# Kernel optimization log

Measured on AMD Instinct MI355X. Metric: run time of the kernel, lower is better.

## Reference

```python
import jax, jax.numpy as jnp
import numpy as np

EPS = 1e-5
K = 16  # neighbors

def bn(x, g, b):
    # BatchNorm in training mode: stats over all axes except the last (channel)
    ax = tuple(range(x.ndim - 1))
    m = x.mean(ax, keepdims=True)
    v = x.var(ax, keepdims=True)
    return g * (x - m) * jax.lax.rsqrt(v + EPS) + b

def setup_inputs() -> dict:
    key = jax.random.key(0)
    ks = jax.random.split(key, 12)
    B, N, M, C, D = 2, 16384, 4096, 32, 64
    H = D // 2
    p = lambda k, s: jax.random.normal(k, s, dtype=jnp.float32) * 0.1
    inp = {}
    inp["xyz"] = jax.random.normal(ks[0], (B, N, 3), dtype=jnp.float32)
    inp["feats"] = jax.random.normal(ks[1], (B, C, N), dtype=jnp.float32)
    inp["sample_idx"] = jax.random.randint(ks[2], (B, M), 0, N, dtype=jnp.int32)
    # RelativePosEncoder mlp: Conv2d(10, H, 1) + BN
    inp["W_pos"] = p(ks[3], (10, H)); inp["b_pos"] = jnp.zeros(H); inp["g_pos"] = jnp.ones(H); inp["be_pos"] = jnp.zeros(H)
    # feature_mlp: Conv2d(C, H, 1) + BN
    inp["W_feat"] = p(ks[4], (C, H)); inp["b_feat"] = jnp.zeros(H); inp["g_feat"] = jnp.ones(H); inp["be_feat"] = jnp.zeros(H)
    # attention score mlp: Conv2d(D, D, 1, bias=False)
    inp["W_score"] = p(ks[5], (D, D))
    # out_mlp: Conv1d(D, D, 1, bias=False) + BN
    inp["W_out"] = p(ks[6], (D, D)); inp["g_out"] = jnp.ones(D); inp["be_out"] = jnp.zeros(D)
    # LFA shortcut: Conv1d(C, D, 1, bias=False) + BN
    inp["W_sc1"] = p(ks[7], (C, D)); inp["g_sc1"] = jnp.ones(D); inp["be_sc1"] = jnp.zeros(D)
    # unit shortcut: Conv1d(C, D, 1, bias=False) + BN
    inp["W_sc2"] = p(ks[8], (C, D)); inp["g_sc2"] = jnp.ones(D); inp["be_sc2"] = jnp.zeros(D)
    return inp

def reference(xyz, feats, sample_idx,
              W_pos, b_pos, g_pos, be_pos,
              W_feat, b_feat, g_feat, be_feat,
              W_score,
              W_out, g_out, be_out,
              W_sc1, g_sc1, be_sc1,
              W_sc2, g_sc2, be_sc2):
    B, C, N = feats.shape
    featsT = jnp.transpose(feats, (0, 2, 1))                    # [B,N,C]
    xyz_ds = jnp.take_along_axis(xyz, sample_idx[:, :, None], axis=1)  # [B,M,3]
    # KNN: squared distances are monotone in cdist -> same topk indices
    d2 = jnp.sum((xyz_ds[:, :, None, :] - xyz[:, None, :, :]) ** 2, axis=-1)  # [B,M,N]
    _, knn_idx = jax.lax.top_k(-d2, K)                           # [B,M,K]
    gather = jax.vmap(lambda pts, idx: pts[idx])
    neigh_xyz = gather(xyz, knn_idx)                             # [B,M,K,3]
    neigh_feats = gather(featsT, knn_idx)                        # [B,M,K,C]
    center_feats = jnp.take_along_axis(featsT, sample_idx[:, :, None], axis=1)  # [B,M,C]
    # relative position encoding
    center = jnp.broadcast_to(xyz_ds[:, :, None, :], neigh_xyz.shape)
    rel = xyz_ds[:, :, None, :] - neigh_xyz                      # [B,M,K,3]
    dist = jnp.linalg.norm(rel, axis=-1, keepdims=True)          # [B,M,K,1]
    posf = jnp.concatenate([center, neigh_xyz, rel, dist], axis=-1)  # [B,M,K,10]
    pos_feats = jax.nn.relu(bn(posf @ W_pos + b_pos, g_pos, be_pos))       # [B,M,K,H]
    feat_feats = jax.nn.relu(bn(neigh_feats @ W_feat + b_feat, g_feat, be_feat))  # [B,M,K,H]
    combined = jnp.concatenate([feat_feats, pos_feats], axis=-1)  # [B,M,K,D]
    # attention pooling: softmax over the K (neighbor) axis
    scores = jax.nn.softmax(combined @ W_score, axis=2)
    pooled = jnp.sum(scores * combined, axis=2)                  # [B,M,D]
    out = jax.nn.relu(bn(pooled @ W_out, g_out, be_out))         # [B,M,D]
    sc1 = bn(jnp.mean(neigh_feats, axis=2) @ W_sc1, g_sc1, be_sc1)
    f_lfa = out + sc1
    f_sc = bn(center_feats @ W_sc2, g_sc2, be_sc2)
    y = jax.nn.relu(f_lfa + f_sc)                                # [B,M,D]
    return xyz_ds, jnp.transpose(y, (0, 2, 1)), sample_idx
```

## Files before the change

kernel.cpp:

```cpp
#include <hip/hip_runtime.h>
#include <math.h>

#define BB 2
#define NN 16384
#define MM 4096
#define C_IN 32
#define D_DIM 64
#define H_DIM 32
#define KNB 16
#define EPSV 1e-5f
#define FLT_BIG 3.0e38f
#define CAPK 128
#define NSPL 4
#define SPTS (NN / NSPL)

#define SPOS_SUM 0
#define SPOS_SQ 32
#define SFEAT_SUM 64
#define SFEAT_SQ 96
#define SSC1_SUM 128
#define SSC1_SQ 192
#define SSC2_SUM 256
#define SSC2_SQ 320
#define SOUT_SUM 384
#define SOUT_SQ 448
#define STATS_LEN 512
#define PA_W 384
#define PB_W 128
#define NBLK (BB * MM / 4)

__device__ __forceinline__ int clampi_r19(int v, int lo, int hi) {
    return v < lo ? lo : (v > hi ? hi : v);
}

__global__ __launch_bounds__(256) void prep_r19(const float* __restrict__ feats,
                                                const float* __restrict__ xyz,
                                                const int* __restrict__ sample_idx,
                                                float* __restrict__ featsT,
                                                float* __restrict__ xyz4,
                                                float* __restrict__ stats,
                                                float* __restrict__ out) {
    __shared__ float tile[C_IN][65];
    const int tid = threadIdx.x;
    const int b = blockIdx.x >> 8;
    const int n0 = (blockIdx.x & 255) * 64;
#pragma unroll
    for (int it = 0; it < 8; ++it) {
        int c = (tid >> 6) + 4 * it;
        int n = tid & 63;
        tile[c][n] = feats[((size_t)b * C_IN + c) * NN + n0 + n];
    }
    int e = blockIdx.x * 256 + tid;
    if (e < STATS_LEN) stats[e] = 0.f;
    if (e < BB * NN) {
        float x = xyz[e * 3 + 0], y = xyz[e * 3 + 1], z = xyz[e * 3 + 2];
        xyz4[e * 4 + 0] = x;
        xyz4[e * 4 + 1] = y;
        xyz4[e * 4 + 2] = z;
        xyz4[e * 4 + 3] = x * x + y * y + z * z;
    }
    if (e < BB * MM) {
        int bb2 = e >> 12;
        int sidx = clampi_r19(sample_idx[e], 0, NN - 1);
        const float* p = xyz + (size_t)(bb2 * NN + sidx) * 3;
        out[e * 3 + 0] = p[0];
        out[e * 3 + 1] = p[1];
        out[e * 3 + 2] = p[2];
        out[BB * MM * 3 + BB * D_DIM * MM + e] = (float)sample_idx[e];
    }
    __syncthreads();
#pragma unroll
    for (int it = 0; it < 8; ++it) {
        int c = tid & 31;
        int nn = (tid >> 5) + 8 * it;
        featsT[((size_t)b * NN + n0 + nn) * C_IN + c] = tile[c][nn];
    }
}

__device__ void knn_fullsplit_r19(const float* __restrict__ base4, int n0,
                                  float m2x, float m2y, float m2z, int lane,
                                  float* __restrict__ outd, int* __restrict__ outi) {
    float d2v[KNB]; int iv[KNB];
#pragma unroll
    for (int i = 0; i < KNB; i++) { d2v[i] = FLT_BIG; iv[i] = 0x7FFFFFFF; }
    float curmax = FLT_BIG; int amax = 0;
    for (int t = 0; t < SPTS / 64; ++t) {
        int n = n0 + lane + t * 64;
        const float4 p = *reinterpret_cast<const float4*>(base4 + (size_t)n * 4);
        float d2 = fmaf(p.x, m2x, p.w);
        d2 = fmaf(p.y, m2y, d2);
        d2 = fmaf(p.z, m2z, d2);
        if (d2 < curmax) {
#pragma unroll
            for (int i = 0; i < KNB; i++)
                if (i == amax) { d2v[i] = d2; iv[i] = n; }
            curmax = d2v[0]; amax = 0;
#pragma unroll
            for (int i = 1; i < KNB; i++)
                if (d2v[i] > curmax) { curmax = d2v[i]; amax = i; }
        }
    }
#pragma unroll
    for (int i = 0; i < KNB; i++) {
#pragma unroll
        for (int j = 0; j < KNB - 1; j++) {
            bool sw = (d2v[j] > d2v[j + 1]) ||
                      (d2v[j] == d2v[j + 1] && iv[j] > iv[j + 1]);
            if (sw) {
                float td = d2v[j]; d2v[j] = d2v[j + 1]; d2v[j + 1] = td;
                int   ti = iv[j];  iv[j]  = iv[j + 1];  iv[j + 1]  = ti;
            }
        }
    }
    float myd = FLT_BIG; int myidx = 0x7FFFFFFF;
#pragma unroll 1
    for (int r = 0; r < KNB; r++) {
        float cv = d2v[0]; int cid = iv[0]; int ml = lane;
#pragma unroll
        for (int off = 32; off > 0; off >>= 1) {
            float ov = __shfl_xor(cv, off);
            int   oid = __shfl_xor(cid, off);
            int   ol = __shfl_xor(ml, off);
            bool take = (ov < cv) || (ov == cv && oid < cid);
            cv = take ? ov : cv; cid = take ? oid : cid; ml = take ? ol : ml;
        }
        if (lane == r) { myd = cv; myidx = cid; }
        if (lane == ml) {
#pragma unroll
            for (int i = 0; i < KNB - 1; i++) { d2v[i] = d2v[i + 1]; iv[i] = iv[i + 1]; }
            d2v[KNB - 1] = FLT_BIG; iv[KNB - 1] = 0x7FFFFFFF;
        }
    }
    if (lane < KNB) { outd[lane] = myd; outi[lane] = myidx; }
}

__global__ __launch_bounds__(256) void knn_r19(const float* __restrict__ xyz4,
                                               const int* __restrict__ sample_idx,
                                               float* __restrict__ cand_d,
                                               int* __restrict__ cand_i) {
    __shared__ float bufd[16][CAPK];
    __shared__ int   bufi[16][CAPK];
    const int tid = threadIdx.x;
    const int w = tid >> 6, lane = tid & 63;
    const int split = blockIdx.x & (NSPL - 1);
    const int qgrp = blockIdx.x >> 2;
    const int qbase = qgrp * 16 + w * 4;
    const int b = qbase >> 12;
    const int n0 = split * SPTS;
    const float* base4 = xyz4 + (size_t)b * NN * 4;
    const float4* p4 = reinterpret_cast<const float4*>(base4) + n0 + lane;

    float m2x[4], m2y[4], m2z[4], md[4], v16[4];
#pragma unroll
    for (int j = 0; j < 4; j++) {
        int s = clampi_r19(sample_idx[qbase + j], 0, NN - 1);
        m2x[j] = -2.f * base4[(size_t)s * 4 + 0];
        m2y[j] = -2.f * base4[(size_t)s * 4 + 1];
        m2z[j] = -2.f * base4[(size_t)s * 4 + 2];
        md[j] = FLT_BIG;
    }
#pragma unroll 8
    for (int it = 0; it < SPTS / 64; ++it) {
        const float4 p = p4[(size_t)it * 64];
#pragma unroll
        for (int j = 0; j < 4; j++) {
            float t = fmaf(p.x, m2x[j], p.w);
            t = fmaf(p.y, m2y[j], t);
            t = fmaf(p.z, m2z[j], t);
            md[j] = fminf(md[j], t);
        }
    }
    {
        float sv[4];
#pragma unroll
        for (int j = 0; j < 4; j++) sv[j] = md[j];
#pragma unroll
        for (int k = 2; k <= 64; k <<= 1) {
#pragma unroll
            for (int j2 = k >> 1; j2 >= 1; j2 >>= 1) {
                const bool want_min = (((lane & j2) == 0) == ((lane & k) == 0));
#pragma unroll
                for (int j = 0; j < 4; j++) {
                    float ov = __shfl_xor(sv[j], j2);
                    float mn = fminf(sv[j], ov);
                    float mx = fmaxf(sv[j], ov);
                    sv[j] = want_min ? mn : mx;
                }
            }
        }
#pragma unroll
        for (int j = 0; j < 4; j++) v16[j] = __shfl(sv[j], KNB - 1);
    }
    int cnt[4] = {0, 0, 0, 0};
#pragma unroll 4
    for (int it = 0; it < SPTS / 64; ++it) {
        const float4 p = p4[(size_t)it * 64];
        const int n = n0 + lane + it * 64;
#pragma unroll
        for (int j = 0; j < 4; j++) {
            float t = fmaf(p.x, m2x[j], p.w);
            t = fmaf(p.y, m2y[j], t);
            t = fmaf(p.z, m2z[j], t);
            bool pred = (t <= v16[j]);
            unsigned long long bal = __ballot(pred);
            if (bal) {
                int pre = __builtin_amdgcn_mbcnt_hi((unsigned)(bal >> 32),
                          __builtin_amdgcn_mbcnt_lo((unsigned)bal, 0u));
                int pos = cnt[j] + pre;
                if (pred && pos < CAPK) {
                    bufd[w * 4 + j][pos] = t;
                    bufi[w * 4 + j][pos] = n;
                }
                cnt[j] += __popcll(bal);
            }
        }
    }
    {
        float dv[4]; int ivv[4];
#pragma unroll
        for (int j = 0; j < 4; j++) {
            const int qi = w * 4 + j;
            bool valid = (cnt[j] <= 64) && (lane < cnt[j]);
            dv[j]  = valid ? bufd[qi][lane] : FLT_BIG;
            ivv[j] = valid ? bufi[qi][lane] : 0x7FFFFFFF;
        }
#pragma unroll
        for (int k = 2; k <= 64; k <<= 1) {
#pragma unroll
            for (int j2 = k >> 1; j2 >= 1; j2 >>= 1) {
                const bool want_min = (((lane & j2) == 0) == ((lane & k) == 0));
#pragma unroll
                for (int j = 0; j < 4; j++) {
                    float od = __shfl_xor(dv[j], j2);
                    int   oi = __shfl_xor(ivv[j], j2);
                    bool mine_less = (dv[j] < od) || (dv[j] == od && ivv[j] < oi);
                    bool keep = (mine_less == want_min);
                    dv[j]  = keep ? dv[j]  : od;
                    ivv[j] = keep ? ivv[j] : oi;
                }
            }
        }
#pragma unroll 1
        for (int j = 0; j < 4; j++) {
            const int qi = w * 4 + j;
            const int q = qbase + j;
            float* outd = cand_d + ((size_t)q * NSPL + split) * KNB;
            int*   outi = cand_i + ((size_t)q * NSPL + split) * KNB;
            if (cnt[j] <= 64) {
                if (lane < KNB) { outd[lane] = dv[j]; outi[lane] = ivv[j]; }
            } else if (cnt[j] <= CAPK) {
#pragma unroll 1
                for (int half = 0; half < 2; ++half) {
                    int i = lane + 64 * half;
                    if (i < cnt[j]) {
                        float di = bufd[qi][i]; int xi = bufi[qi][i];
                        int rank = 0;
                        for (int t = 0; t < cnt[j]; ++t) {
                            float dt = bufd[qi][t]; int xt = bufi[qi][t];
                            rank += (dt < di || (dt == di && xt < xi)) ? 1 : 0;
                        }
                        if (rank < KNB) { outd[rank] = di; outi[rank] = xi; }
                    }
                }
            } else {
                knn_fullsplit_r19(base4, n0, m2x[j], m2y[j], m2z[j], lane, outd, outi);
            }
        }
    }
}

__device__ __forceinline__ void prebn_r19(const float (*posf)[12], const float (*nf)[C_IN],
                                          int k, int h,
                                          const float* __restrict__ W_pos, const float* __restrict__ b_pos,
                                          const float* __restrict__ W_feat, const float* __restrict__ b_feat,
                                          float* a_out, float* f_out) {
    float4 p0 = *reinterpret_cast<const float4*>(&posf[k][0]);
    float4 p1 = *reinterpret_cast<const float4*>(&posf[k][4]);
    float p8 = posf[k][8], p9 = posf[k][9];
    float a = b_pos[h];
    a += p0.x * W_pos[0 * H_DIM + h]; a += p0.y * W_pos[1 * H_DIM + h];
    a += p0.z * W_pos[2 * H_DIM + h]; a += p0.w * W_pos[3 * H_DIM + h];
    a += p1.x * W_pos[4 * H_DIM + h]; a += p1.y * W_pos[5 * H_DIM + h];
    a += p1.z * W_pos[6 * H_DIM + h]; a += p1.w * W_pos[7 * H_DIM + h];
    a += p8 * W_pos[8 * H_DIM + h];   a += p9 * W_pos[9 * H_DIM + h];
    float f = b_feat[h];
#pragma unroll
    for (int j4 = 0; j4 < C_IN / 4; ++j4) {
        float4 c = *reinterpret_cast<const float4*>(&nf[k][j4 * 4]);
        f += c.x * W_feat[(j4 * 4 + 0) * H_DIM + h];
        f += c.y * W_feat[(j4 * 4 + 1) * H_DIM + h];
        f += c.z * W_feat[(j4 * 4 + 2) * H_DIM + h];
        f += c.w * W_feat[(j4 * 4 + 3) * H_DIM + h];
    }
    *a_out = a; *f_out = f;
}

__global__ __launch_bounds__(256) void stageA_r19(const float* __restrict__ xyz4,
                                                  const int* __restrict__ sample_idx,
                                                  const float* __restrict__ featsT,
                                                  const float* __restrict__ cand_d,
                                                  const int* __restrict__ cand_i,
                                                  const float* __restrict__ W_pos, const float* __restrict__ b_pos,
                                                  const float* __restrict__ W_feat, const float* __restrict__ b_feat,
                                                  const float* __restrict__ W_sc1, const float* __restrict__ W_sc2,
                                                  float* __restrict__ combpre,
                                                  float* __restrict__ sc1_pre, float* __restrict__ sc2_pre,
                                                  float* __restrict__ partialsA) {
    __shared__ int   idxs[4][KNB];
    __shared__ float sd[4][64];
    __shared__ int   si[4][64];
    __shared__ __align__(16) float posf[4][KNB][12];
    __shared__ __align__(16) float nf[4][KNB][C_IN];
    __shared__ float meanf[4][C_IN];
    __shared__ float centerf[4][C_IN];
    __shared__ float posS[4][H_DIM], posQ[4][H_DIM], featS[4][H_DIM], featQ[4][H_DIM];
    __shared__ float s1S[4][D_DIM], s1Q[4][D_DIM], s2S[4][D_DIM], s2Q[4][D_DIM];
    const int tid = threadIdx.x;
    const int w = tid >> 6, lane = tid & 63;
    const int q = blockIdx.x * 4 + w;
    const int b = q >> 12;
    const int sidx = clampi_r19(sample_idx[q], 0, NN - 1);
    const float* base4 = xyz4 + (size_t)b * NN * 4;

    float d = cand_d[(size_t)q * 64 + lane];
    int   i = cand_i[(size_t)q * 64 + lane];
    float qx = base4[(size_t)sidx * 4 + 0];
    float qy = base4[(size_t)sidx * 4 + 1];
    float qz = base4[(size_t)sidx * 4 + 2];
    float cfv = 0.f;
    if (lane < C_IN) cfv = featsT[((size_t)b * NN + sidx) * C_IN + lane];

    {
        sd[w][lane] = d; si[w][lane] = i;
        __syncthreads();
        int rank = 0;
#pragma unroll
        for (int t = 0; t < 64; ++t) {
            float dt = sd[w][t]; int it = si[w][t];
            rank += (dt < d || (dt == d && it < i)) ? 1 : 0;
        }
        if (rank < KNB) idxs[w][rank] = i;
        if (lane < C_IN) centerf[w][lane] = cfv;
        __syncthreads();
    }

    if (lane < KNB) {
        int idx = clampi_r19(idxs[w][lane], 0, NN - 1);
        float nx = base4[(size_t)idx * 4 + 0];
        float ny = base4[(size_t)idx * 4 + 1];
        float nz = base4[(size_t)idx * 4 + 2];
        float rx = qx - nx, ry = qy - ny, rz = qz - nz;
        float dist = sqrtf(rx * rx + ry * ry + rz * rz);
        posf[w][lane][0] = qx; posf[w][lane][1] = qy; posf[w][lane][2] = qz;
        posf[w][lane][3] = nx; posf[w][lane][4] = ny; posf[w][lane][5] = nz;
        posf[w][lane][6] = rx; posf[w][lane][7] = ry; posf[w][lane][8] = rz;
        posf[w][lane][9] = dist; posf[w][lane][10] = 0.f; posf[w][lane][11] = 0.f;
    }
    __syncthreads();
    const float* fT = featsT + (size_t)b * NN * C_IN;
#pragma unroll
    for (int ii = 0; ii < 2; ++ii) {
        int e4 = lane + 64 * ii;
        int k = e4 >> 3, c4 = e4 & 7;
        const float4 v = *reinterpret_cast<const float4*>(fT + (size_t)idxs[w][k] * C_IN + c4 * 4);
        *reinterpret_cast<float4*>(&nf[w][k][c4 * 4]) = v;
    }
    __syncthreads();

    const int h = lane & 31;
    float sP = 0.f, qP = 0.f, sF = 0.f, qF = 0.f;
    float* cp = combpre + (size_t)q * (KNB * D_DIM);
#pragma unroll
    for (int i2 = 0; i2 < 8; i2++) {
        int k = ((lane + 64 * i2) >> 5);
        float a, f;
        prebn_r19(posf[w], nf[w], k, h, W_pos, b_pos, W_feat, b_feat, &a, &f);
        sP += a; qP += a * a;
        sF += f; qF += f * f;
        cp[k * D_DIM + h] = f;
        cp[k * D_DIM + H_DIM + h] = a;
    }
    sP += __shfl_xor(sP, 32); qP += __shfl_xor(qP, 32);
    sF += __shfl_xor(sF, 32); qF += __shfl_xor(qF, 32);
    if (lane < H_DIM) {
        posS[w][h] = sP; posQ[w][h] = qP; featS[w][h] = sF; featQ[w][h] = qF;
    }
    if (lane < C_IN) {
        float s = 0.f;
#pragma unroll
        for (int k = 0; k < KNB; k++) s += nf[w][k][lane];
        meanf[w][lane] = s * (1.f / (float)KNB);
    }
    __syncthreads();
    {
        float a = 0.f, c2 = 0.f;
#pragma unroll
        for (int j = 0; j < C_IN; j++) {
            a  += meanf[w][j]   * W_sc1[j * D_DIM + lane];
            c2 += centerf[w][j] * W_sc2[j * D_DIM + lane];
        }
        sc1_pre[(size_t)q * D_DIM + lane] = a;
        sc2_pre[(size_t)q * D_DIM + lane] = c2;
        s1S[w][lane] = a;  s1Q[w][lane] = a * a;
        s2S[w][lane] = c2; s2Q[w][lane] = c2 * c2;
    }
    __syncthreads();
    float* row = partialsA + (size_t)blockIdx.x * PA_W;
    if (tid < H_DIM) {
        row[SPOS_SUM + tid]  = posS[0][tid] + posS[1][tid] + posS[2][tid] + posS[3][tid];
        row[SPOS_SQ + tid]   = posQ[0][tid] + posQ[1][tid] + posQ[2][tid] + posQ[3][tid];
        row[SFEAT_SUM + tid] = featS[0][tid] + featS[1][tid] + featS[2][tid] + featS[3][tid];
        row[SFEAT_SQ + tid]  = featQ[0][tid] + featQ[1][tid] + featQ[2][tid] + featQ[3][tid];
    } else if (tid >= 64 && tid < 128) {
        int dd = tid - 64;
        row[SSC1_SUM + dd] = s1S[0][dd] + s1S[1][dd] + s1S[2][dd] + s1S[3][dd];
        row[SSC1_SQ + dd]  = s1Q[0][dd] + s1Q[1][dd] + s1Q[2][dd] + s1Q[3][dd];
    } else if (tid >= 128 && tid < 192) {
        int dd = tid - 128;
        row[SSC2_SUM + dd] = s2S[0][dd] + s2S[1][dd] + s2S[2][dd] + s2S[3][dd];
        row[SSC2_SQ + dd]  = s2Q[0][dd] + s2Q[1][dd] + s2Q[2][dd] + s2Q[3][dd];
    }
}

#define NRSPLIT 64
__global__ __launch_bounds__(256) void reduce_r19(const float* __restrict__ partials,
                                                  int rows, int width,
                                                  float* __restrict__ stats_out) {
    const int wchunks = (width + 255) / 256;
    const int wi = blockIdx.x % wchunks;
    const int pi = blockIdx.x / wchunks;
    const int c = wi * 256 + threadIdx.x;
    if (c >= width) return;
    const int per = rows / NRSPLIT;
    const int p0 = pi * per;
    float s = 0.f;
    for (int p = p0; p < p0 + per; ++p) s += partials[(size_t)p * width + c];
    atomicAdd(&stats_out[c], s);
}

__global__ __launch_bounds__(256) void stageB_r19(const float* __restrict__ combpre,
                                                  const float* __restrict__ g_pos, const float* __restrict__ be_pos,
                                                  const float* __restrict__ g_feat, const float* __restrict__ be_feat,
                                                  const float* __restrict__ W_score, const float* __restrict__ W_out,
                                                  const float* __restrict__ stats,
                                                  float* __restrict__ out_pre,
                                                  float* __restrict__ partialsB) {
    __shared__ __align__(16) float comb[4][KNB][D_DIM];
    __shared__ float scl[D_DIM], shf[D_DIM];
    __shared__ float pooled[4][D_DIM];
    __shared__ float oS[4][D_DIM], oQ[4][D_DIM];
    const int tid = threadIdx.x;
    const int w = tid >> 6, lane = tid & 63;
    const int q = blockIdx.x * 4 + w;

    if (tid < D_DIM) {
        const float inv1 = 1.f / (float)(BB * MM * KNB);
        float mean, var, g, bb;
        if (tid < H_DIM) {
            mean = stats[SFEAT_SUM + tid] * inv1;
            var  = fmaxf(stats[SFEAT_SQ + tid] * inv1 - mean * mean, 0.f);
            g = g_feat[tid]; bb = be_feat[tid];
        } else {
            int h = tid - H_DIM;
            mean = stats[SPOS_SUM + h] * inv1;
            var  = fmaxf(stats[SPOS_SQ + h] * inv1 - mean * mean, 0.f);
            g = g_pos[h]; bb = be_pos[h];
        }
        float s = g * rsqrtf(var + EPSV);
        scl[tid] = s;
        shf[tid] = bb - mean * s;
    }
    __syncthreads();

    const float4* src = reinterpret_cast<const float4*>(combpre + (size_t)blockIdx.x * 4 * KNB * D_DIM);
#pragma unroll
    for (int i = 0; i < 4; ++i) {
        int f = tid + 256 * i;
        int qloc = f >> 8;
        int k = (f >> 4) & 15;
        int j4 = f & 15;
        float4 v = src[f];
        int j = j4 * 4;
        v.x = fmaxf(v.x * scl[j + 0] + shf[j + 0], 0.f);
        v.y = fmaxf(v.y * scl[j + 1] + shf[j + 1], 0.f);
        v.z = fmaxf(v.z * scl[j + 2] + shf[j + 2], 0.f);
        v.w = fmaxf(v.w * scl[j + 3] + shf[j + 3], 0.f);
        *reinterpret_cast<float4*>(&comb[qloc][k][j]) = v;
    }
    __syncthreads();

    const int d = lane;
    float s[KNB];
#pragma unroll
    for (int k = 0; k < KNB; k++) s[k] = 0.f;
#pragma unroll 4
    for (int j4 = 0; j4 < D_DIM / 4; ++j4) {
        float w0 = W_score[(j4 * 4 + 0) * D_DIM + d];
        float w1 = W_score[(j4 * 4 + 1) * D_DIM + d];
        float w2 = W_score[(j4 * 4 + 2) * D_DIM + d];
        float w3 = W_score[(j4 * 4 + 3) * D_DIM + d];
#pragma unroll
        for (int k = 0; k < KNB; k++) {
            float4 cb = *reinterpret_cast<const float4*>(&comb[w][k][j4 * 4]);
            s[k] += cb.x * w0 + cb.y * w1 + cb.z * w2 + cb.w * w3;
        }
    }
    float mx = s[0];
#pragma unroll
    for (int k = 1; k < KNB; k++) mx = fmaxf(mx, s[k]);
    float sum = 0.f;
#pragma unroll
    for (int k = 0; k < KNB; k++) { s[k] = __expf(s[k] - mx); sum += s[k]; }
    float inv = 1.f / sum;
    float pv = 0.f;
#pragma unroll
    for (int k = 0; k < KNB; k++) pv += s[k] * inv * comb[w][k][d];
    pooled[w][d] = pv;
    __syncthreads();
    float o = 0.f;
#pragma unroll
    for (int dd = 0; dd < D_DIM; dd++) o += pooled[w][dd] * W_out[dd * D_DIM + d];
    out_pre[(size_t)q * D_DIM + d] = o;
    oS[w][d] = o; oQ[w][d] = o * o;
    __syncthreads();
    float* row = partialsB + (size_t)blockIdx.x * PB_W;
    if (tid < D_DIM) {
        row[tid] = oS[0][tid] + oS[1][tid] + oS[2][tid] + oS[3][tid];
    } else if (tid < 2 * D_DIM) {
        int dd = tid - D_DIM;
        row[D_DIM + dd] = oQ[0][dd] + oQ[1][dd] + oQ[2][dd] + oQ[3][dd];
    }
}

__global__ __launch_bounds__(256) void final_r19(const float* __restrict__ out_pre,
                                                 const float* __restrict__ sc1_pre,
                                                 const float* __restrict__ sc2_pre,
                                                 const float* __restrict__ stats,
                                                 const float* __restrict__ g_out, const float* __restrict__ be_out,
                                                 const float* __restrict__ g_sc1, const float* __restrict__ be_sc1,
                                                 const float* __restrict__ g_sc2, const float* __restrict__ be_sc2,
                                                 float* __restrict__ out) {
    __shared__ float yt[64][65];
    const int tid = threadIdx.x;
    const int blk = blockIdx.x;
    const int b = blk >> 6;
    const int m0 = (blk & 63) * 64;
    const int d = tid & 63;

    const float invn = 1.f / (float)(BB * MM);
    float mo = stats[SOUT_SUM + d] * invn;
    float vo = fmaxf(stats[SOUT_SQ + d] * invn - mo * mo, 0.f);
    float so = g_out[d] * rsqrtf(vo + EPSV);
    float oo = be_out[d] - mo * so;
    float m1 = stats[SSC1_SUM + d] * invn;
    float v1 = fmaxf(stats[SSC1_SQ + d] * invn - m1 * m1, 0.f);
    float s1 = g_sc1[d] * rsqrtf(v1 + EPSV);
    float o1 = be_sc1[d] - m1 * s1;
    float m2 = stats[SSC2_SUM + d] * invn;
    float v2 = fmaxf(stats[SSC2_SQ + d] * invn - m2 * m2, 0.f);
    float s2 = g_sc2[d] * rsqrtf(v2 + EPSV);
    float o2 = be_sc2[d] - m2 * s2;

#pragma unroll
    for (int p = 0; p < 16; p++) {
        int ml = (tid >> 6) + 4 * p;
        size_t q = (size_t)b * MM + m0 + ml;
        float x_out = fmaxf(out_pre[q * D_DIM + d] * so + oo, 0.f);
        float x1 = sc1_pre[q * D_DIM + d] * s1 + o1;
        float x2 = sc2_pre[q * D_DIM + d] * s2 + o2;
        yt[ml][d] = fmaxf(x_out + x1 + x2, 0.f);
    }
    __syncthreads();
#pragma unroll
    for (int p = 0; p < 16; p++) {
        int dr = (tid >> 6) + 4 * p;
        int mc = tid & 63;
        out[BB * MM * 3 + (size_t)b * (D_DIM * MM) + (size_t)dr * MM + m0 + mc] = yt[mc][dr];
    }
}

extern "C" void kernel_launch(void* const* d_in, const int* in_sizes, int n_in,
                              void* d_out, int out_size, void* d_ws, size_t ws_size,
                              hipStream_t stream) {
    const float* xyz        = (const float*)d_in[0];
    const float* feats      = (const float*)d_in[1];
    const int*   sample_idx = (const int*)d_in[2];
    const float* W_pos  = (const float*)d_in[3];
    const float* b_pos  = (const float*)d_in[4];
    const float* g_pos  = (const float*)d_in[5];
    const float* be_pos = (const float*)d_in[6];
    const float* W_feat  = (const float*)d_in[7];
    const float* b_feat  = (const float*)d_in[8];
    const float* g_feat  = (const float*)d_in[9];
    const float* be_feat = (const float*)d_in[10];
    const float* W_score = (const float*)d_in[11];
    const float* W_out  = (const float*)d_in[12];
    const float* g_out  = (const float*)d_in[13];
    const float* be_out = (const float*)d_in[14];
    const float* W_sc1  = (const float*)d_in[15];
    const float* g_sc1  = (const float*)d_in[16];
    const float* be_sc1 = (const float*)d_in[17];
    const float* W_sc2  = (const float*)d_in[18];
    const float* g_sc2  = (const float*)d_in[19];
    const float* be_sc2 = (const float*)d_in[20];

    float* out = (float*)d_out;
    float* ws = (float*)d_ws;

    float* featsT    = ws;
    float* xyz4      = featsT + 1048576;
    float* sc1_pre   = xyz4 + 131072;
    float* sc2_pre   = sc1_pre + 524288;
    float* out_pre   = sc2_pre + 524288;
    float* stats     = out_pre + 524288;
    float* partialsA = stats + STATS_LEN;
    float* partialsB = partialsA + NBLK * PA_W;
    float* cand_d    = partialsB + NBLK * PB_W;
    int*   cand_i    = (int*)(cand_d + (size_t)BB * MM * NSPL * KNB);
    float* combpre   = (float*)(cand_i + (size_t)BB * MM * NSPL * KNB);

    prep_r19<<<BB * (NN / 64), 256, 0, stream>>>(feats, xyz, sample_idx,
                                                 featsT, xyz4, stats, out);

    knn_r19<<<(BB * MM / 16) * NSPL, 256, 0, stream>>>(xyz4, sample_idx, cand_d, cand_i);

    stageA_r19<<<NBLK, 256, 0, stream>>>(xyz4, sample_idx, featsT, cand_d, cand_i,
                                         W_pos, b_pos, W_feat, b_feat, W_sc1, W_sc2,
                                         combpre, sc1_pre, sc2_pre, partialsA);
    reduce_r19<<<2 * NRSPLIT, 256, 0, stream>>>(partialsA, NBLK, PA_W, stats);

    stageB_r19<<<NBLK, 256, 0, stream>>>(combpre,
                                         g_pos, be_pos, g_feat, be_feat,
                                         W_score, W_out, stats, out_pre, partialsB);
    reduce_r19<<<1 * NRSPLIT, 256, 0, stream>>>(partialsB, NBLK, PB_W, stats + SOUT_SUM);

    final_r19<<<BB * (MM / 64), 256, 0, stream>>>(out_pre, sc1_pre, sc2_pre, stats,
                                                  g_out, be_out, g_sc1, be_sc1, g_sc2, be_sc2, out);
}
```

Measured before the change: 251.9 us.

## Use packed float2 math in KNN and MLPs, replace rank-merge with bitonic shuffle

Adds a pair-interleaved xyz layout, stored in the combpre workspace, so the KNN distance scan and candidate filter handle two points per lane using packed float2 FMA. stageA swaps the shared-memory O(64) rank selection of 16 neighbours out of 4 sorted runs for a wave-level bitonic merge via shuffles. It also drops several __syncthreads, caches W_pos/W_feat in registers as float2 pairs, and packs the stageB score matmul into float2 FMAs. Risks: the xyz8 buffer aliases combpre, the removed barriers may break cross-wave shared-memory reads, and the ballot ordering now differs for candidate collection.

```diff
diff --git a/kernel.cpp b/kernel.cpp
--- a/kernel.cpp
+++ b/kernel.cpp
@@ -29,15 +29,22 @@
 #define PB_W 128
 #define NBLK (BB * MM / 4)
 
-__device__ __forceinline__ int clampi_r19(int v, int lo, int hi) {
+typedef float f32x2 __attribute__((ext_vector_type(2)));
+
+__device__ __forceinline__ f32x2 mk2_r20(float a, float b) {
+    f32x2 r; r.x = a; r.y = b; return r;
+}
+
+__device__ __forceinline__ int clampi_r20(int v, int lo, int hi) {
     return v < lo ? lo : (v > hi ? hi : v);
 }
 
-__global__ __launch_bounds__(256) void prep_r19(const float* __restrict__ feats,
+__global__ __launch_bounds__(256) void prep_r20(const float* __restrict__ feats,
                                                 const float* __restrict__ xyz,
                                                 const int* __restrict__ sample_idx,
                                                 float* __restrict__ featsT,
                                                 float* __restrict__ xyz4,
+                                                float* __restrict__ xyz8,
                                                 float* __restrict__ stats,
                                                 float* __restrict__ out) {
     __shared__ float tile[C_IN][65];
@@ -54,14 +61,20 @@
     if (e < STATS_LEN) stats[e] = 0.f;
     if (e < BB * NN) {
         float x = xyz[e * 3 + 0], y = xyz[e * 3 + 1], z = xyz[e * 3 + 2];
+        float w = x * x + y * y + z * z;
         xyz4[e * 4 + 0] = x;
         xyz4[e * 4 + 1] = y;
         xyz4[e * 4 + 2] = z;
-        xyz4[e * 4 + 3] = x * x + y * y + z * z;
+        xyz4[e * 4 + 3] = w;
+        size_t pb = ((size_t)(e >> 1)) * 8 + (e & 1);
+        xyz8[pb + 0] = x;
+        xyz8[pb + 2] = y;
+        xyz8[pb + 4] = z;
+        xyz8[pb + 6] = w;
     }
     if (e < BB * MM) {
         int bb2 = e >> 12;
-        int sidx = clampi_r19(sample_idx[e], 0, NN - 1);
+        int sidx = clampi_r20(sample_idx[e], 0, NN - 1);
         const float* p = xyz + (size_t)(bb2 * NN + sidx) * 3;
         out[e * 3 + 0] = p[0];
         out[e * 3 + 1] = p[1];
@@ -77,7 +90,7 @@
     }
 }
 
-__device__ void knn_fullsplit_r19(const float* __restrict__ base4, int n0,
+__device__ void knn_fullsplit_r20(const float* __restrict__ base4, int n0,
                                   float m2x, float m2y, float m2z, int lane,
                                   float* __restrict__ outd, int* __restrict__ outi) {
     float d2v[KNB]; int iv[KNB];
@@ -134,7 +147,8 @@
     if (lane < KNB) { outd[lane] = myd; outi[lane] = myidx; }
 }
 
-__global__ __launch_bounds__(256) void knn_r19(const float* __restrict__ xyz4,
+__global__ __launch_bounds__(256) void knn_r20(const float* __restrict__ xyz4,
+                                               const float* __restrict__ xyz8,
                                                const int* __restrict__ sample_idx,
                                                float* __restrict__ cand_d,
                                                int* __restrict__ cand_i) {
@@ -148,28 +162,39 @@
     const int b = qbase >> 12;
     const int n0 = split * SPTS;
     const float* base4 = xyz4 + (size_t)b * NN * 4;
-    const float4* p4 = reinterpret_cast<const float4*>(base4) + n0 + lane;
-
-    float m2x[4], m2y[4], m2z[4], md[4], v16[4];
+    const float* base8 = xyz8 + (size_t)b * NN * 4;
+    const float4* q8 = reinterpret_cast<const float4*>(base8) + ((size_t)(n0 >> 1) + lane) * 2;
+
+    f32x2 m2x2[4], m2y2[4], m2z2[4], md2[4];
+    float md[4], v16[4];
 #pragma unroll
     for (int j = 0; j < 4; j++) {
-        int s = clampi_r19(sample_idx[qbase + j], 0, NN - 1);
-        m2x[j] = -2.f * base4[(size_t)s * 4 + 0];
-        m2y[j] = -2.f * base4[(size_t)s * 4 + 1];
-        m2z[j] = -2.f * base4[(size_t)s * 4 + 2];
-        md[j] = FLT_BIG;
-    }
-#pragma unroll 8
-    for (int it = 0; it < SPTS / 64; ++it) {
-        const float4 p = p4[(size_t)it * 64];
+        int s = clampi_r20(sample_idx[qbase + j], 0, NN - 1);
+        float mx = -2.f * base4[(size_t)s * 4 + 0];
+        float my = -2.f * base4[(size_t)s * 4 + 1];
+        float mz = -2.f * base4[(size_t)s * 4 + 2];
+        m2x2[j] = mk2_r20(mx, mx);
+        m2y2[j] = mk2_r20(my, my);
+        m2z2[j] = mk2_r20(mz, mz);
+        md2[j] = mk2_r20(FLT_BIG, FLT_BIG);
+    }
+#pragma unroll 4
+    for (int it = 0; it < SPTS / 128; ++it) {
+        const float4 A = q8[(size_t)it * 128];
+        const float4 B = q8[(size_t)it * 128 + 1];
+        f32x2 x2 = mk2_r20(A.x, A.y), y2 = mk2_r20(A.z, A.w);
+        f32x2 z2 = mk2_r20(B.x, B.y), w2 = mk2_r20(B.z, B.w);
 #pragma unroll
         for (int j = 0; j < 4; j++) {
-            float t = fmaf(p.x, m2x[j], p.w);
-            t = fmaf(p.y, m2y[j], t);
-            t = fmaf(p.z, m2z[j], t);
-            md[j] = fminf(md[j], t);
-        }
-    }
+            f32x2 t2 = x2 * m2x2[j] + w2;
+            t2 = y2 * m2y2[j] + t2;
+            t2 = z2 * m2z2[j] + t2;
+            md2[j].x = fminf(md2[j].x, t2.x);
+            md2[j].y = fminf(md2[j].y, t2.y);
+        }
+    }
+#pragma unroll
+    for (int j = 0; j < 4; j++) md[j] = fminf(md2[j].x, md2[j].y);
     {
         float sv[4];
 #pragma unroll
@@ -193,25 +218,31 @@
     }
     int cnt[4] = {0, 0, 0, 0};
 #pragma unroll 4
-    for (int it = 0; it < SPTS / 64; ++it) {
-        const float4 p = p4[(size_t)it * 64];
-        const int n = n0 + lane + it * 64;
+    for (int it = 0; it < SPTS / 128; ++it) {
+        const float4 A = q8[(size_t)it * 128];
+        const float4 B = q8[(size_t)it * 128 + 1];
+        f32x2 x2 = mk2_r20(A.x, A.y), y2 = mk2_r20(A.z, A.w);
+        f32x2 z2 = mk2_r20(B.x, B.y), w2 = mk2_r20(B.z, B.w);
+        const int ne = n0 + (it << 7) + (lane << 1);
 #pragma unroll
         for (int j = 0; j < 4; j++) {
-            float t = fmaf(p.x, m2x[j], p.w);
-            t = fmaf(p.y, m2y[j], t);
-            t = fmaf(p.z, m2z[j], t);
-            bool pred = (t <= v16[j]);
-            unsigned long long bal = __ballot(pred);
-            if (bal) {
-                int pre = __builtin_amdgcn_mbcnt_hi((unsigned)(bal >> 32),
-                          __builtin_amdgcn_mbcnt_lo((unsigned)bal, 0u));
-                int pos = cnt[j] + pre;
-                if (pred && pos < CAPK) {
-                    bufd[w * 4 + j][pos] = t;
-                    bufi[w * 4 + j][pos] = n;
-                }
-                cnt[j] += __popcll(bal);
+            f32x2 t2 = x2 * m2x2[j] + w2;
+            t2 = y2 * m2y2[j] + t2;
+            t2 = z2 * m2z2[j] + t2;
+            bool h0 = (t2.x <= v16[j]);
+            bool h1 = (t2.y <= v16[j]);
+            unsigned long long b0 = __ballot(h0);
+            unsigned long long b1 = __ballot(h1);
+            if (b0 | b1) {
+                int base = cnt[j];
+                int c0 = __popcll(b0);
+                int p0 = base + __builtin_amdgcn_mbcnt_hi((unsigned)(b0 >> 32),
+                             __builtin_amdgcn_mbcnt_lo((unsigned)b0, 0u));
+                int p1 = base + c0 + __builtin_amdgcn_mbcnt_hi((unsigned)(b1 >> 32),
+                             __builtin_amdgcn_mbcnt_lo((unsigned)b1, 0u));
+                if (h0 && p0 < CAPK) { bufd[w * 4 + j][p0] = t2.x; bufi[w * 4 + j][p0] = ne; }
+                if (h1 && p1 < CAPK) { bufd[w * 4 + j][p1] = t2.y; bufi[w * 4 + j][p1] = ne + 1; }
+                cnt[j] = base + c0 + __popcll(b1);
             }
         }
     }
@@ -263,39 +294,33 @@
                     }
                 }
             } else {
-                knn_fullsplit_r19(base4, n0, m2x[j], m2y[j], m2z[j], lane, outd, outi);
+                float mx = m2x2[j].x, my = m2y2[j].x, mz = m2z2[j].x;
+                knn_fullsplit_r20(base4, n0, mx, my, mz, lane, outd, outi);
             }
         }
     }
 }
 
-__device__ __forceinline__ void prebn_r19(const float (*posf)[12], const float (*nf)[C_IN],
-                                          int k, int h,
-                                          const float* __restrict__ W_pos, const float* __restrict__ b_pos,
-                                          const float* __restrict__ W_feat, const float* __restrict__ b_feat,
+__device__ __forceinline__ void prebn_r20(const float (*posf)[12], const float (*nf)[C_IN],
+                                          int k,
+                                          const f32x2* __restrict__ wp2, float bp,
+                                          const f32x2* __restrict__ wf2, float bf,
                                           float* a_out, float* f_out) {
-    float4 p0 = *reinterpret_cast<const float4*>(&posf[k][0]);
-    float4 p1 = *reinterpret_cast<const float4*>(&posf[k][4]);
-    float p8 = posf[k][8], p9 = posf[k][9];
-    float a = b_pos[h];
-    a += p0.x * W_pos[0 * H_DIM + h]; a += p0.y * W_pos[1 * H_DIM + h];
-    a += p0.z * W_pos[2 * H_DIM + h]; a += p0.w * W_pos[3 * H_DIM + h];
-    a += p1.x * W_pos[4 * H_DIM + h]; a += p1.y * W_pos[5 * H_DIM + h];
-    a += p1.z * W_pos[6 * H_DIM + h]; a += p1.w * W_pos[7 * H_DIM + h];
-    a += p8 * W_pos[8 * H_DIM + h];   a += p9 * W_pos[9 * H_DIM + h];
-    float f = b_feat[h];
-#pragma unroll
-    for (int j4 = 0; j4 < C_IN / 4; ++j4) {
-        float4 c = *reinterpret_cast<const float4*>(&nf[k][j4 * 4]);
-        f += c.x * W_feat[(j4 * 4 + 0) * H_DIM + h];
-        f += c.y * W_feat[(j4 * 4 + 1) * H_DIM + h];
-        f += c.z * W_feat[(j4 * 4 + 2) * H_DIM + h];
-        f += c.w * W_feat[(j4 * 4 + 3) * H_DIM + h];
-    }
-    *a_out = a; *f_out = f;
-}
-
-__global__ __launch_bounds__(256) void stageA_r19(const float* __restrict__ xyz4,
+    const f32x2* pp = reinterpret_cast<const f32x2*>(&posf[k][0]);
+    f32x2 a2 = pp[0] * wp2[0];
+    a2 = pp[1] * wp2[1] + a2;
+    a2 = pp[2] * wp2[2] + a2;
+    a2 = pp[3] * wp2[3] + a2;
+    a2 = pp[4] * wp2[4] + a2;
+    const f32x2* nn2 = reinterpret_cast<const f32x2*>(&nf[k][0]);
+    f32x2 f2 = nn2[0] * wf2[0];
+#pragma unroll
+    for (int t = 1; t < 16; ++t) f2 = nn2[t] * wf2[t] + f2;
+    *a_out = bp + a2.x + a2.y;
+    *f_out = bf + f2.x + f2.y;
+}
+
+__global__ __launch_bounds__(256) void stageA_r20(const float* __restrict__ xyz4,
                                                   const int* __restrict__ sample_idx,
                                                   const float* __restrict__ featsT,
                                                   const float* __restrict__ cand_d,
@@ -306,9 +331,6 @@
                                                   float* __restrict__ combpre,
                                                   float* __restrict__ sc1_pre, float* __restrict__ sc2_pre,
                                                   float* __restrict__ partialsA) {
-    __shared__ int   idxs[4][KNB];
-    __shared__ float sd[4][64];
-    __shared__ int   si[4][64];
     __shared__ __align__(16) float posf[4][KNB][12];
     __shared__ __align__(16) float nf[4][KNB][C_IN];
     __shared__ float meanf[4][C_IN];
@@ -319,33 +341,36 @@
     const int w = tid >> 6, lane = tid & 63;
     const int q = blockIdx.x * 4 + w;
     const int b = q >> 12;
-    const int sidx = clampi_r19(sample_idx[q], 0, NN - 1);
+    const int sidx = clampi_r20(sample_idx[q], 0, NN - 1);
     const float* base4 = xyz4 + (size_t)b * NN * 4;
 
-    float d = cand_d[(size_t)q * 64 + lane];
-    int   i = cand_i[(size_t)q * 64 + lane];
+    float dmv; int imv;
+    {
+        const int run = lane >> 4, pos = lane & 15;
+        const int ridx = (run & 1) ? (15 - pos) : pos;
+        dmv = cand_d[(size_t)q * 64 + run * 16 + ridx];
+        imv = cand_i[(size_t)q * 64 + run * 16 + ridx];
+    }
     float qx = base4[(size_t)sidx * 4 + 0];
     float qy = base4[(size_t)sidx * 4 + 1];
     float qz = base4[(size_t)sidx * 4 + 2];
-    float cfv = 0.f;
-    if (lane < C_IN) cfv = featsT[((size_t)b * NN + sidx) * C_IN + lane];
-
-    {
-        sd[w][lane] = d; si[w][lane] = i;
-        __syncthreads();
-        int rank = 0;
-#pragma unroll
-        for (int t = 0; t < 64; ++t) {
-            float dt = sd[w][t]; int it = si[w][t];
-            rank += (dt < d || (dt == d && it < i)) ? 1 : 0;
-        }
-        if (rank < KNB) idxs[w][rank] = i;
-        if (lane < C_IN) centerf[w][lane] = cfv;
-        __syncthreads();
+    if (lane < C_IN) centerf[w][lane] = featsT[((size_t)b * NN + sidx) * C_IN + lane];
+#pragma unroll
+    for (int k = 32; k <= 64; k <<= 1) {
+#pragma unroll
+        for (int j2 = k >> 1; j2 >= 1; j2 >>= 1) {
+            const bool want_min = (((lane & j2) == 0) == ((lane & k) == 0));
+            float od = __shfl_xor(dmv, j2);
+            int   oi = __shfl_xor(imv, j2);
+            bool mine_less = (dmv < od) || (dmv == od && imv < oi);
+            bool keep = (mine_less == want_min);
+            dmv = keep ? dmv : od;
+            imv = keep ? imv : oi;
+        }
     }
 
     if (lane < KNB) {
-        int idx = clampi_r19(idxs[w][lane], 0, NN - 1);
+        int idx = clampi_r20(imv, 0, NN - 1);
         float nx = base4[(size_t)idx * 4 + 0];
         float ny = base4[(size_t)idx * 4 + 1];
         float nz = base4[(size_t)idx * 4 + 2];
@@ -356,25 +381,33 @@
         posf[w][lane][6] = rx; posf[w][lane][7] = ry; posf[w][lane][8] = rz;
         posf[w][lane][9] = dist; posf[w][lane][10] = 0.f; posf[w][lane][11] = 0.f;
     }
-    __syncthreads();
     const float* fT = featsT + (size_t)b * NN * C_IN;
 #pragma unroll
     for (int ii = 0; ii < 2; ++ii) {
         int e4 = lane + 64 * ii;
         int k = e4 >> 3, c4 = e4 & 7;
-        const float4 v = *reinterpret_cast<const float4*>(fT + (size_t)idxs[w][k] * C_IN + c4 * 4);
+        int idx = clampi_r20(__shfl(imv, k), 0, NN - 1);
+        const float4 v = *reinterpret_cast<const float4*>(fT + (size_t)idx * C_IN + c4 * 4);
         *reinterpret_cast<float4*>(&nf[w][k][c4 * 4]) = v;
     }
-    __syncthreads();
 
     const int h = lane & 31;
+    f32x2 wp2[5], wf2[16];
+#pragma unroll
+    for (int t = 0; t < 5; ++t)
+        wp2[t] = mk2_r20(W_pos[(2 * t) * H_DIM + h], W_pos[(2 * t + 1) * H_DIM + h]);
+#pragma unroll
+    for (int t = 0; t < 16; ++t)
+        wf2[t] = mk2_r20(W_feat[(2 * t) * H_DIM + h], W_feat[(2 * t + 1) * H_DIM + h]);
+    const float bp = b_pos[h], bf = b_feat[h];
+
     float sP = 0.f, qP = 0.f, sF = 0.f, qF = 0.f;
     float* cp = combpre + (size_t)q * (KNB * D_DIM);
 #pragma unroll
     for (int i2 = 0; i2 < 8; i2++) {
         int k = ((lane + 64 * i2) >> 5);
         float a, f;
-        prebn_r19(posf[w], nf[w], k, h, W_pos, b_pos, W_feat, b_feat, &a, &f);
+        prebn_r20(posf[w], nf[w], k, wp2, bp, wf2, bf, &a, &f);
         sP += a; qP += a * a;
         sF += f; qF += f * f;
         cp[k * D_DIM + h] = f;
@@ -391,7 +424,6 @@
         for (int k = 0; k < KNB; k++) s += nf[w][k][lane];
         meanf[w][lane] = s * (1.f / (float)KNB);
     }
-    __syncthreads();
     {
         float a = 0.f, c2 = 0.f;
 #pragma unroll
@@ -423,7 +455,7 @@
 }
 
 #define NRSPLIT 64
-__global__ __launch_bounds__(256) void reduce_r19(const float* __restrict__ partials,
+__global__ __launch_bounds__(256) void reduce_r20(const float* __restrict__ partials,
                                                   int rows, int width,
                                                   float* __restrict__ stats_out) {
     const int wchunks = (width + 255) / 256;
@@ -438,7 +470,7 @@
     atomicAdd(&stats_out[c], s);
 }
 
-__global__ __launch_bounds__(256) void stageB_r19(const float* __restrict__ combpre,
+__global__ __launch_bounds__(256) void stageB_r20(const float* __restrict__ combpre,
                                                   const float* __restrict__ g_pos, const float* __restrict__ be_pos,
                                                   const float* __restrict__ g_feat, const float* __restrict__ be_feat,
                                                   const float* __restrict__ W_score, const float* __restrict__ W_out,
@@ -490,21 +522,25 @@
     __syncthreads();
 
     const int d = lane;
-    float s[KNB];
-#pragma unroll
-    for (int k = 0; k < KNB; k++) s[k] = 0.f;
+    f32x2 s2[KNB];
+#pragma unroll
+    for (int k = 0; k < KNB; k++) s2[k] = mk2_r20(0.f, 0.f);
 #pragma unroll 4
     for (int j4 = 0; j4 < D_DIM / 4; ++j4) {
-        float w0 = W_score[(j4 * 4 + 0) * D_DIM + d];
-        float w1 = W_score[(j4 * 4 + 1) * D_DIM + d];
-        float w2 = W_score[(j4 * 4 + 2) * D_DIM + d];
-        float w3 = W_score[(j4 * 4 + 3) * D_DIM + d];
+        f32x2 wA = mk2_r20(W_score[(j4 * 4 + 0) * D_DIM + d],
+                           W_score[(j4 * 4 + 1) * D_DIM + d]);
+        f32x2 wB = mk2_r20(W_score[(j4 * 4 + 2) * D_DIM + d],
+                           W_score[(j4 * 4 + 3) * D_DIM + d]);
 #pragma unroll
         for (int k = 0; k < KNB; k++) {
-            float4 cb = *reinterpret_cast<const float4*>(&comb[w][k][j4 * 4]);
-            s[k] += cb.x * w0 + cb.y * w1 + cb.z * w2 + cb.w * w3;
-        }
-    }
+            const f32x2* cb = reinterpret_cast<const f32x2*>(&comb[w][k][j4 * 4]);
+            s2[k] = cb[0] * wA + s2[k];
+            s2[k] = cb[1] * wB + s2[k];
+        }
+    }
+    float s[KNB];
+#pragma unroll
+    for (int k = 0; k < KNB; k++) s[k] = s2[k].x + s2[k].y;
     float mx = s[0];
 #pragma unroll
     for (int k = 1; k < KNB; k++) mx = fmaxf(mx, s[k]);
@@ -532,7 +568,7 @@
     }
 }
 
-__global__ __launch_bounds__(256) void final_r19(const float* __restrict__ out_pre,
+__global__ __launch_bounds__(256) void final_r20(const float* __restrict__ out_pre,
                                                  const float* __restrict__ sc1_pre,
                                                  const float* __restrict__ sc2_pre,
                                                  const float* __restrict__ stats,
@@ -618,22 +654,23 @@
     float* cand_d    = partialsB + NBLK * PB_W;
     int*   cand_i    = (int*)(cand_d + (size_t)BB * MM * NSPL * KNB);
     float* combpre   = (float*)(cand_i + (size_t)BB * MM * NSPL * KNB);
-
-    prep_r19<<<BB * (NN / 64), 256, 0, stream>>>(feats, xyz, sample_idx,
-                                                 featsT, xyz4, stats, out);
-
-    knn_r19<<<(BB * MM / 16) * NSPL, 256, 0, stream>>>(xyz4, sample_idx, cand_d, cand_i);
-
-    stageA_r19<<<NBLK, 256, 0, stream>>>(xyz4, sample_idx, featsT, cand_d, cand_i,
+    float* xyz8      = combpre;
+
+    prep_r20<<<BB * (NN / 64), 256, 0, stream>>>(feats, xyz, sample_idx,
+                                                 featsT, xyz4, xyz8, stats, out);
+
+    knn_r20<<<(BB * MM / 16) * NSPL, 256, 0, stream>>>(xyz4, xyz8, sample_idx, cand_d, cand_i);
+
+    stageA_r20<<<NBLK, 256, 0, stream>>>(xyz4, sample_idx, featsT, cand_d, cand_i,
                                          W_pos, b_pos, W_feat, b_feat, W_sc1, W_sc2,
                                          combpre, sc1_pre, sc2_pre, partialsA);
-    reduce_r19<<<2 * NRSPLIT, 256, 0, stream>>>(partialsA, NBLK, PA_W, stats);
-
-    stageB_r19<<<NBLK, 256, 0, stream>>>(combpre,
+    reduce_r20<<<2 * NRSPLIT, 256, 0, stream>>>(partialsA, NBLK, PA_W, stats);
+
+    stageB_r20<<<NBLK, 256, 0, stream>>>(combpre,
                                          g_pos, be_pos, g_feat, be_feat,
                                          W_score, W_out, stats, out_pre, partialsB);
-    reduce_r19<<<1 * NRSPLIT, 256, 0, stream>>>(partialsB, NBLK, PB_W, stats + SOUT_SUM);
-
-    final_r19<<<BB * (MM / 64), 256, 0, stream>>>(out_pre, sc1_pre, sc2_pre, stats,
+    reduce_r20<<<1 * NRSPLIT, 256, 0, stream>>>(partialsB, NBLK, PB_W, stats + SOUT_SUM);
+
+    final_r20<<<BB * (MM / 64), 256, 0, stream>>>(out_pre, sc1_pre, sc2_pre, stats,
                                                   g_out, be_out, g_sc1, be_sc1, g_sc2, be_sc2, out);
 }
```

Result: faster. 235.6 us (-6.5%).
